# Performance work log

Measured on AMD Instinct MI355X. Metric: run time of the kernel, lower is better.

## Reference

```python
import jax, jax.numpy as jnp
import numpy as np

H = 12       # num heads
D = 64       # head dim
EPS = 1e-5

def rms_norm(x, eps=EPS):
    var = jnp.mean(jnp.square(x), axis=-1, keepdims=True)
    return x * jax.lax.rsqrt(var + eps)

def rotate_half(x):
    x1, x2 = jnp.split(x, 2, axis=-1)
    return jnp.concatenate([-x2, x1], axis=-1)

def setup_inputs() -> dict:
    key = jax.random.key(0)
    ks = jax.random.split(key, 7)
    B, S, C = 2, 2048, 768
    inter = 2048
    hidden_states = jax.random.normal(ks[0], (B, S, C), dtype=jnp.float32)
    # RoPE tables (cos/sin over positions, standard half-duplicated freqs)
    theta = 10000.0
    inv_freq = 1.0 / (theta ** (jnp.arange(0, D, 2, dtype=jnp.float32) / D))
    t = jnp.arange(S, dtype=jnp.float32)
    freqs = jnp.outer(t, inv_freq)            # [S, D/2]
    emb = jnp.concatenate([freqs, freqs], -1)  # [S, D]
    cos = jnp.cos(emb)
    sin = jnp.sin(emb)
    s = 0.02
    w_qkv = jax.random.normal(ks[1], (3 * H * D, C), dtype=jnp.float32) * s
    w_o = jax.random.normal(ks[2], (C, H * D), dtype=jnp.float32) * s
    w_gate_up = jax.random.normal(ks[3], (2 * inter, C), dtype=jnp.float32) * s
    w_down = jax.random.normal(ks[4], (C, inter), dtype=jnp.float32) * s
    return {"hidden_states": hidden_states, "cos": cos, "sin": sin,
            "w_qkv": w_qkv, "w_o": w_o, "w_gate_up": w_gate_up, "w_down": w_down}

def reference(hidden_states, cos, sin, w_qkv, w_o, w_gate_up, w_down):
    B, S, C = hidden_states.shape
    scale = 1.0 / jnp.sqrt(jnp.asarray(D, hidden_states.dtype))
    # ----- attention (manual, non-flash) -----
    qkv = jnp.einsum('bsc,ec->bse', hidden_states, w_qkv)
    qkv = qkv.reshape(B, S, 3 * H, D)
    q, k, v = qkv[:, :, :H], qkv[:, :, H:2 * H], qkv[:, :, 2 * H:]
    c = cos[None, :, None, :]
    sn = sin[None, :, None, :]
    q = q * c + rotate_half(q) * sn
    k = k * c + rotate_half(k) * sn
    scores = jnp.einsum('bihd,bjhd->bhij', q, k) * scale  # [B,H,S,S]
    attn = jax.nn.softmax(scores, axis=-1)
    ctx = jnp.einsum('bhij,bjhd->bihd', attn, v).reshape(B, S, H * D)
    attn_out = jnp.einsum('bse,ce->bsc', ctx, w_o)
    x = rms_norm(hidden_states + attn_out)
    # ----- SwiGLU MLP -----
    gu = jnp.einsum('bsc,ec->bse', x, w_gate_up)
    gate, up = jnp.split(gu, 2, axis=-1)
    mlp_out = jnp.einsum('bsi,ci->bsc', jax.nn.silu(gate) * up, w_down)
    return rms_norm(x + mlp_out)
```

## Files before the change

### kernel.cpp

```cpp
#include <hip/hip_runtime.h>


typedef __attribute__((ext_vector_type(8))) __bf16 bf16x8;
typedef __attribute__((ext_vector_type(8))) short short8;
typedef __attribute__((ext_vector_type(4))) short short4v;
typedef __attribute__((ext_vector_type(4))) float f32x4;
typedef __attribute__((ext_vector_type(4))) float float4v;
typedef __attribute__((ext_vector_type(4))) unsigned int u32x4;

#define CDIM   768
#define HEADS  12
#define DH     64
#define SEQ    2048
#define BATCH  2
#define MROWS  4096
#define QKV_N  2304
#define INTER  2048
#define GU_N   4096
#define NSPLIT 4
#define KCHUNK (SEQ / NSPLIT)
#define BH     (BATCH * HEADS)

#define QSCALE 0.18033688011112043f

static __device__ __forceinline__ unsigned short f2bf(float f) {
  unsigned int u = __builtin_bit_cast(unsigned int, f);
  u += 0x7fffu + ((u >> 16) & 1u);
  return (unsigned short)(u >> 16);
}
static __device__ __forceinline__ float bf2f(unsigned short u) {
  return __builtin_bit_cast(float, ((unsigned int)u) << 16);
}

static __device__ __forceinline__ bf16x8 ld8(const unsigned short* p) {
  return __builtin_bit_cast(bf16x8, *reinterpret_cast<const short8*>(p));
}

static __device__ __forceinline__ float exp2_raw(float x) {
  float r; asm("v_exp_f32 %0, %1" : "=v"(r) : "v"(x)); return r;
}
static __device__ __forceinline__ unsigned cvtpk(float lo, float hi) {
  unsigned r;
  asm("v_cvt_pk_bf16_f32 %0, %1, %2" : "=v"(r) : "v"(lo), "v"(hi));
  return r;
}

static __device__ __forceinline__ void pl32swap(unsigned& a, unsigned& b) {
  auto r = __builtin_amdgcn_permlane32_swap(a, b, false, false);
  a = r[0]; b = r[1];
}
static __device__ __forceinline__ void pl16swap(unsigned& a, unsigned& b) {
  auto r = __builtin_amdgcn_permlane16_swap(a, b, false, false);
  a = r[0]; b = r[1];
}
static __device__ __forceinline__ float red32max(float x) {
  unsigned xi = __builtin_bit_cast(unsigned, x);
  auto r = __builtin_amdgcn_permlane32_swap(xi, xi, false, false);
  return fmaxf(__builtin_bit_cast(float, r[0]), __builtin_bit_cast(float, r[1]));
}
static __device__ __forceinline__ float red16max(float x) {
  unsigned xi = __builtin_bit_cast(unsigned, x);
  auto r = __builtin_amdgcn_permlane16_swap(xi, xi, false, false);
  return fmaxf(__builtin_bit_cast(float, r[0]), __builtin_bit_cast(float, r[1]));
}
static __device__ __forceinline__ float red32sum(float x) {
  unsigned xi = __builtin_bit_cast(unsigned, x);
  auto r = __builtin_amdgcn_permlane32_swap(xi, xi, false, false);
  return __builtin_bit_cast(float, r[0]) + __builtin_bit_cast(float, r[1]);
}
static __device__ __forceinline__ float red16sum(float x) {
  unsigned xi = __builtin_bit_cast(unsigned, x);
  auto r = __builtin_amdgcn_permlane16_swap(xi, xi, false, false);
  return __builtin_bit_cast(float, r[0]) + __builtin_bit_cast(float, r[1]);
}

__global__ __launch_bounds__(256) void cast_all(
    const float* __restrict__ h, const float* __restrict__ wqkv,
    const float* __restrict__ wo, const float* __restrict__ wgu,
    const float* __restrict__ wd,
    unsigned short* __restrict__ hb, unsigned short* __restrict__ wqkvb,
    unsigned short* __restrict__ wob, unsigned short* __restrict__ wgub,
    unsigned short* __restrict__ wdb) {
  const int n0 = 786432, n1 = 442368, n2 = 147456, n3 = 786432, n4 = 393216;
  const int total = n0 + n1 + n2 + n3 + n4;
  for (int i = blockIdx.x * blockDim.x + threadIdx.x; i < total;
       i += gridDim.x * blockDim.x) {
    int j = i;
    const float* src; unsigned short* dst;
    if      (j < n0)            { src = h;    dst = hb;    }
    else if ((j -= n0) < n1)    { src = wqkv; dst = wqkvb; }
    else if ((j -= n1) < n2)    { src = wo;   dst = wob;   }
    else if ((j -= n2) < n3)    { src = wgu;  dst = wgub;  }
    else    { j -= n3;            src = wd;   dst = wdb;   }
    float4v v = *reinterpret_cast<const float4v*>(src + 4 * (size_t)j);
    short4v o;
#pragma unroll
    for (int e = 0; e < 4; ++e) o[e] = (short)f2bf(v[e]);
    *reinterpret_cast<short4v*>(dst + 4 * (size_t)j) = o;
  }
}

template <int BN, bool BF16OUT>
__global__ __launch_bounds__(256) void gemm_lds(
    const unsigned short* __restrict__ A, const unsigned short* __restrict__ W,
    void* __restrict__ Cout, int Mm, int Nn, int Kk) {
  constexpr int MR = (BN == 128) ? 4 : 2;
  __shared__ unsigned short Alds[4096];
  __shared__ unsigned short Blds[BN * 32];
  const int t = threadIdx.x;
  const int lane = t & 63, w = t >> 6;
  const int lr = lane & 15, lg = lane >> 4;
  const int row0 = blockIdx.y * 128, col0 = blockIdx.x * BN;
  const int wrb = (BN == 128) ? (w >> 1) * 64 : w * 32;
  const int wcb = (BN == 128) ? (w & 1) * 64 : 0;

  const unsigned short* ga = A + (size_t)(row0 + (t >> 2)) * Kk + (t & 3) * 8;
  const unsigned short* gb = W + (size_t)(col0 + (t >> 2)) * Kk + (t & 3) * 8;
  const size_t g64 = (size_t)64 * Kk;
  unsigned short* la0 = Alds + w * 512;
  unsigned short* lb0 = Blds + w * 512;
  const unsigned short* ra = Alds + (wrb + lr) * 32 + lg * 8;
  const unsigned short* rb = Blds + (wcb + lr) * 32 + lg * 8;

  f32x4 acc[MR][4] = {};
  for (int k0 = 0; k0 < Kk; k0 += 32) {
    __builtin_amdgcn_global_load_lds((const unsigned int*)(ga + k0),
                                     (unsigned int*)la0, 16, 0, 0);
    __builtin_amdgcn_global_load_lds((const unsigned int*)(ga + k0 + g64),
                                     (unsigned int*)(la0 + 2048), 16, 0, 0);
    __builtin_amdgcn_global_load_lds((const unsigned int*)(gb + k0),
                                     (unsigned int*)lb0, 16, 0, 0);
    if constexpr (BN == 128)
      __builtin_amdgcn_global_load_lds((const unsigned int*)(gb + k0 + g64),
                                       (unsigned int*)(lb0 + 2048), 16, 0, 0);
    __syncthreads();
    bf16x8 af[MR], bfr[4];
#pragma unroll
    for (int m = 0; m < MR; ++m) af[m] = ld8(ra + m * 512);
#pragma unroll
    for (int n = 0; n < 4; ++n) bfr[n] = ld8(rb + n * 512);
    __builtin_amdgcn_s_setprio(1);
#pragma unroll
    for (int m = 0; m < MR; ++m)
#pragma unroll
      for (int n = 0; n < 4; ++n)
        acc[m][n] = __builtin_amdgcn_mfma_f32_16x16x32_bf16(af[m], bfr[n],
                                                            acc[m][n], 0, 0, 0);
    __builtin_amdgcn_s_setprio(0);
    __syncthreads();
  }
#pragma unroll
  for (int m = 0; m < MR; ++m)
#pragma unroll
    for (int j = 0; j < 4; ++j) {
      const size_t roff = (size_t)(row0 + wrb + m * 16 + lg * 4 + j) * Nn +
                          col0 + wcb + lr;
      if constexpr (BF16OUT) {
        unsigned short* cr = (unsigned short*)Cout + roff;
#pragma unroll
        for (int n = 0; n < 4; ++n) cr[n * 16] = f2bf(acc[m][n][j]);
      } else {
        float* cr = (float*)Cout + roff;
#pragma unroll
        for (int n = 0; n < 4; ++n) cr[n * 16] = acc[m][n][j];
      }
    }
}

__global__ __launch_bounds__(256) void rope_qk(
    const unsigned short* __restrict__ qkv, const float* __restrict__ cosT,
    const float* __restrict__ sinT, unsigned short* __restrict__ qtile,
    unsigned short* __restrict__ ktile) {
  const int row = blockIdx.x * 4 + (threadIdx.x >> 6);
  const int d = threadIdx.x & 63;
  const int hh = row % 24;
  const int bs = row / 24;
  const int s = bs & (SEQ - 1);
  const int b = bs >> 11;
  float v = bf2f(qkv[(size_t)bs * QKV_N + hh * 64 + d]);
  float partner = __shfl_xor(v, 32, 64);
  float rot = (d < 32) ? -partner : partner;
  v = v * cosT[s * 64 + d] + rot * sinT[s * 64 + d];
  const int t = s >> 4, lr = s & 15;
  const int dh = d >> 5, lg = (d & 31) >> 3, j = d & 7;
  if (hh < 12) {
    const int bh = b * HEADS + hh;
    qtile[((size_t)(bh * 128 + t) * 2 + dh) * 512 + (lg * 16 + lr) * 8 + j] =
        f2bf(v * QSCALE);
  } else {
    const int bh = b * HEADS + (hh - 12);
    ktile[((size_t)(bh * 128 + t) * 2 + dh) * 512 + (lg * 16 + lr) * 8 + j] =
        f2bf(v);
  }
}

__global__ __launch_bounds__(256) void v_trans(
    const unsigned short* __restrict__ qkv, unsigned short* __restrict__ vT) {
  __shared__ unsigned short tile[64][66];
  const int bh = blockIdx.x;
  const int s0 = blockIdx.y * 64;
  const int b = bh / HEADS, h = bh % HEADS;
  const unsigned short* src = qkv + ((size_t)(b * SEQ + s0)) * QKV_N + (24 + h) * 64;
  const int d = threadIdx.x & 63, sg = threadIdx.x >> 6;
#pragma unroll
  for (int i = 0; i < 16; ++i) {
    int s = sg * 16 + i;
    tile[s][d] = src[(size_t)s * QKV_N + d];
  }
  __syncthreads();
  const int lane = threadIdx.x & 63, wid = threadIdx.x >> 6;
  const int lr = lane & 15, lg = lane >> 4;
  unsigned short* dst = vT + ((size_t)bh * 64 + (s0 >> 5)) * 4 * 512;
#pragma unroll
  for (int tt = 0; tt < 2; ++tt) {
    const int ti = wid * 2 + tt;
    const int kt = ti >> 2, d0 = (ti & 3) * 16;
    short8 o;
#pragma unroll
    for (int j = 0; j < 8; ++j)
      o[j] = (short)tile[kt * 32 + lg * 8 + j][d0 + lr];
    *reinterpret_cast<short8*>(dst + ((size_t)kt * 4 + (ti & 3)) * 512 +
                               lane * 8) = o;
  }
}

__global__ __launch_bounds__(256) void attn_fused(
    const unsigned short* __restrict__ qtile, const unsigned short* __restrict__ ktile,
    const unsigned short* __restrict__ vtile, unsigned short* __restrict__ ctxp,
    float2* __restrict__ ml) {
  const int lane = threadIdx.x & 63, wid = threadIdx.x >> 6;
  const int tid = blockIdx.x * 4 + wid;
  const int sp = tid & 3;
  const int qt = (tid >> 2) & 127;
  const int bh = tid >> 9;
  const int lr = lane & 15, lg = lane >> 4;

  const unsigned short* qp =
      qtile + ((size_t)(bh * 128 + qt) * 2) * 512 + lane * 8;
  bf16x8 qf0 = ld8(qp);
  bf16x8 qf1 = ld8(qp + 512);
  const unsigned short* kb = ktile + (size_t)bh * 128 * 2 * 512 + lane * 8;
  const unsigned short* vb = vtile + (size_t)bh * 64 * 4 * 512 + lane * 8;

  f32x4 acc0 = {0,0,0,0}, acc1 = {0,0,0,0}, acc2 = {0,0,0,0}, acc3 = {0,0,0,0};
  float m = -1e30f, l_lane = 0.f;

  for (int k0 = sp * KCHUNK; k0 < sp * KCHUNK + KCHUNK; k0 += 64) {
    const unsigned short* kp = kb + (size_t)(k0 >> 4) * 1024;
    f32x4 st0 = {0,0,0,0}, st1 = {0,0,0,0}, st2 = {0,0,0,0}, st3 = {0,0,0,0};
    __builtin_amdgcn_s_setprio(1);
    st0 = __builtin_amdgcn_mfma_f32_16x16x32_bf16(ld8(kp),        qf0, st0, 0,0,0);
    st0 = __builtin_amdgcn_mfma_f32_16x16x32_bf16(ld8(kp + 512),  qf1, st0, 0,0,0);
    st1 = __builtin_amdgcn_mfma_f32_16x16x32_bf16(ld8(kp + 1024), qf0, st1, 0,0,0);
    st1 = __builtin_amdgcn_mfma_f32_16x16x32_bf16(ld8(kp + 1536), qf1, st1, 0,0,0);
    st2 = __builtin_amdgcn_mfma_f32_16x16x32_bf16(ld8(kp + 2048), qf0, st2, 0,0,0);
    st2 = __builtin_amdgcn_mfma_f32_16x16x32_bf16(ld8(kp + 2560), qf1, st2, 0,0,0);
    st3 = __builtin_amdgcn_mfma_f32_16x16x32_bf16(ld8(kp + 3072), qf0, st3, 0,0,0);
    st3 = __builtin_amdgcn_mfma_f32_16x16x32_bf16(ld8(kp + 3584), qf1, st3, 0,0,0);
    __builtin_amdgcn_s_setprio(0);

    float tmax = fmaxf(
        fmaxf(fmaxf(fmaxf(st0[0], st0[1]), fmaxf(st0[2], st0[3])),
              fmaxf(fmaxf(st1[0], st1[1]), fmaxf(st1[2], st1[3]))),
        fmaxf(fmaxf(fmaxf(st2[0], st2[1]), fmaxf(st2[2], st2[3])),
              fmaxf(fmaxf(st3[0], st3[1]), fmaxf(st3[2], st3[3]))));
    tmax = red16max(red32max(tmax));

    if (tmax > m + 11.0f) {
      float fac = exp2_raw(m - tmax);
      m = tmax;
      l_lane *= fac;
      acc0 *= fac; acc1 *= fac; acc2 *= fac; acc3 *= fac;
    }

    float p[16];
#pragma unroll
    for (int r = 0; r < 4; ++r) {
      p[r]      = exp2_raw(st0[r] - m);
      p[4 + r]  = exp2_raw(st1[r] - m);
      p[8 + r]  = exp2_raw(st2[r] - m);
      p[12 + r] = exp2_raw(st3[r] - m);
    }
    l_lane += (((p[0] + p[1]) + (p[2] + p[3])) +
               ((p[4] + p[5]) + (p[6] + p[7]))) +
              (((p[8] + p[9]) + (p[10] + p[11])) +
               ((p[12] + p[13]) + (p[14] + p[15])));

    unsigned c0 = cvtpk(p[0], p[1]),   c1 = cvtpk(p[2], p[3]);
    unsigned c2 = cvtpk(p[4], p[5]),   c3 = cvtpk(p[6], p[7]);
    unsigned c4 = cvtpk(p[8], p[9]),   c5 = cvtpk(p[10], p[11]);
    unsigned c6 = cvtpk(p[12], p[13]), c7 = cvtpk(p[14], p[15]);
    pl32swap(c0, c2); pl32swap(c1, c3); pl16swap(c0, c2); pl16swap(c1, c3);
    pl32swap(c4, c6); pl32swap(c5, c7); pl16swap(c4, c6); pl16swap(c5, c7);
    u32x4 pw0 = {c0, c1, c2, c3};
    u32x4 pw1 = {c4, c5, c6, c7};
    bf16x8 pf0 = __builtin_bit_cast(bf16x8, pw0);
    bf16x8 pf1 = __builtin_bit_cast(bf16x8, pw1);

    const unsigned short* vp = vb + (size_t)(k0 >> 5) * 2048;
    __builtin_amdgcn_s_setprio(1);
    acc0 = __builtin_amdgcn_mfma_f32_16x16x32_bf16(ld8(vp),        pf0, acc0, 0,0,0);
    acc1 = __builtin_amdgcn_mfma_f32_16x16x32_bf16(ld8(vp + 512),  pf0, acc1, 0,0,0);
    acc2 = __builtin_amdgcn_mfma_f32_16x16x32_bf16(ld8(vp + 1024), pf0, acc2, 0,0,0);
    acc3 = __builtin_amdgcn_mfma_f32_16x16x32_bf16(ld8(vp + 1536), pf0, acc3, 0,0,0);
    acc0 = __builtin_amdgcn_mfma_f32_16x16x32_bf16(ld8(vp + 2048), pf1, acc0, 0,0,0);
    acc1 = __builtin_amdgcn_mfma_f32_16x16x32_bf16(ld8(vp + 2560), pf1, acc1, 0,0,0);
    acc2 = __builtin_amdgcn_mfma_f32_16x16x32_bf16(ld8(vp + 3072), pf1, acc2, 0,0,0);
    acc3 = __builtin_amdgcn_mfma_f32_16x16x32_bf16(ld8(vp + 3584), pf1, acc3, 0,0,0);
    __builtin_amdgcn_s_setprio(0);
  }

  const float l = red16sum(red32sum(l_lane));

  unsigned short* pp = ctxp +
      (((size_t)(sp * BH + bh)) * SEQ + qt * 16 + lr) * DH + 4 * lg;
  short4v o0, o1, o2, o3;
#pragma unroll
  for (int r = 0; r < 4; ++r) {
    o0[r] = (short)f2bf(acc0[r]);
    o1[r] = (short)f2bf(acc1[r]);
    o2[r] = (short)f2bf(acc2[r]);
    o3[r] = (short)f2bf(acc3[r]);
  }
  *reinterpret_cast<short4v*>(pp)      = o0;
  *reinterpret_cast<short4v*>(pp + 16) = o1;
  *reinterpret_cast<short4v*>(pp + 32) = o2;
  *reinterpret_cast<short4v*>(pp + 48) = o3;
  if (lane < 16) {
    float2 v; v.x = m; v.y = l;
    ml[(size_t)sp * (BH * SEQ) + bh * SEQ + qt * 16 + lr] = v;
  }
}

__global__ __launch_bounds__(256) void attn_combine(
    const unsigned short* __restrict__ ctxp, const float2* __restrict__ ml,
    unsigned short* __restrict__ ctx) {
  const int idx = blockIdx.x * 256 + threadIdx.x;
  const int d = idx & 63;
  const int row = idx >> 6;
  float m0 = ml[row].x,                 l0 = ml[row].y;
  float m1 = ml[row + BH*SEQ].x,        l1 = ml[row + BH*SEQ].y;
  float m2 = ml[row + 2*BH*SEQ].x,      l2 = ml[row + 2*BH*SEQ].y;
  float m3 = ml[row + 3*BH*SEQ].x,      l3 = ml[row + 3*BH*SEQ].y;
  float M = fmaxf(fmaxf(m0, m1), fmaxf(m2, m3));
  float w0 = exp2_raw(m0 - M), w1 = exp2_raw(m1 - M);
  float w2 = exp2_raw(m2 - M), w3 = exp2_raw(m3 - M);
  float den = w0 * l0 + w1 * l1 + w2 * l2 + w3 * l3;
  const size_t pstride = (size_t)BH * SEQ * DH;
  float num = w0 * bf2f(ctxp[(size_t)row * DH + d]) +
              w1 * bf2f(ctxp[(size_t)row * DH + d + pstride]) +
              w2 * bf2f(ctxp[(size_t)row * DH + d + 2 * pstride]) +
              w3 * bf2f(ctxp[(size_t)row * DH + d + 3 * pstride]);
  const int bh = row >> 11, s = row & (SEQ - 1);
  const int b = bh / HEADS, h = bh % HEADS;
  ctx[((size_t)(b * SEQ + s)) * CDIM + h * DH + d] = f2bf(num / den);
}

__global__ __launch_bounds__(256) void add_rmsnorm(
    const float* __restrict__ a, const float* __restrict__ b,
    float* __restrict__ outf, unsigned short* __restrict__ outb) {
  const int row = blockIdx.x;
  const int tid = threadIdx.x;
  const float* ap = a + (size_t)row * CDIM;
  const float* bp = b + (size_t)row * CDIM;
  float v0 = ap[tid]       + bp[tid];
  float v1 = ap[tid + 256] + bp[tid + 256];
  float v2 = ap[tid + 512] + bp[tid + 512];
  float ss = v0 * v0 + v1 * v1 + v2 * v2;
#pragma unroll
  for (int off = 32; off > 0; off >>= 1) ss += __shfl_xor(ss, off, 64);
  __shared__ float red[4];
  if ((tid & 63) == 0) red[tid >> 6] = ss;
  __syncthreads();
  float tot = red[0] + red[1] + red[2] + red[3];
  float r = rsqrtf(tot * (1.f / 768.f) + 1e-5f);
  float* of = outf + (size_t)row * CDIM;
  of[tid]       = v0 * r;
  of[tid + 256] = v1 * r;
  of[tid + 512] = v2 * r;
  if (outb) {
    unsigned short* ob = outb + (size_t)row * CDIM;
    ob[tid]       = f2bf(v0 * r);
    ob[tid + 256] = f2bf(v1 * r);
    ob[tid + 512] = f2bf(v2 * r);
  }
}

__global__ __launch_bounds__(256) void silu_mul(
    const unsigned short* __restrict__ gu, unsigned short* __restrict__ hb) {
  const int i = blockIdx.x * 256 + threadIdx.x;
  const int s = i >> 11, c = i & (INTER - 1);
  float g = bf2f(gu[(size_t)s * GU_N + c]);
  float u = bf2f(gu[(size_t)s * GU_N + INTER + c]);
  float sig = 1.f / (1.f + __expf(-g));
  hb[i] = f2bf(g * sig * u);
}

extern "C" void kernel_launch(void* const* d_in, const int* in_sizes, int n_in,
                              void* d_out, int out_size, void* d_ws, size_t ws_size,
                              hipStream_t stream) {
  const float* hidden = (const float*)d_in[0];
  const float* cosT   = (const float*)d_in[1];
  const float* sinT   = (const float*)d_in[2];
  const float* wqkv   = (const float*)d_in[3];
  const float* wo     = (const float*)d_in[4];
  const float* wgu    = (const float*)d_in[5];
  const float* wd     = (const float*)d_in[6];
  float* out = (float*)d_out;

  char* wsp = (char*)d_ws;
  size_t off = 0;
  auto alloc = [&](size_t bytes) { void* p = wsp + off; off += bytes; return p; };

  unsigned short* wqkvb = (unsigned short*)alloc(2ull * 1769472);
  unsigned short* wob   = (unsigned short*)alloc(2ull * 589824);
  unsigned short* wgub  = (unsigned short*)alloc(2ull * 3145728);
  unsigned short* wdb   = (unsigned short*)alloc(2ull * 1572864);
  unsigned short* hb    = (unsigned short*)alloc(2ull * 3145728);
  float*          x     = (float*)alloc(4ull * 3145728);
  unsigned short* xb    = (unsigned short*)alloc(2ull * 3145728);
  const size_t roff = off;

  unsigned short* qkvb = (unsigned short*)alloc(2ull * MROWS * QKV_N);
  unsigned short* qT   = (unsigned short*)alloc(2ull * MROWS * CDIM);
  unsigned short* kT   = (unsigned short*)alloc(2ull * MROWS * CDIM);
  unsigned short* vTb  = (unsigned short*)alloc(2ull * MROWS * CDIM);
  unsigned short* ctx  = (unsigned short*)alloc(2ull * MROWS * CDIM);
  float*          attn = (float*)alloc(4ull * MROWS * CDIM);
  unsigned short* ctxp = (unsigned short*)alloc(2ull * NSPLIT * BH * SEQ * DH);
  float2*         ml   = (float2*)alloc(8ull * NSPLIT * BH * SEQ);

  off = roff;
  unsigned short* gub  = (unsigned short*)alloc(2ull * MROWS * GU_N);
  unsigned short* hmid = (unsigned short*)alloc(2ull * MROWS * INTER);
  float*          mlp  = (float*)alloc(4ull * MROWS * CDIM);
  (void)ws_size; (void)in_sizes; (void)n_in; (void)out_size;

  cast_all<<<2048, 256, 0, stream>>>(hidden, wqkv, wo, wgu, wd,
                                     hb, wqkvb, wob, wgub, wdb);
  gemm_lds<128, true><<<dim3(QKV_N / 128, MROWS / 128), 256, 0, stream>>>(
      hb, wqkvb, qkvb, MROWS, QKV_N, CDIM);
  rope_qk<<<(MROWS * 24) / 4, 256, 0, stream>>>(qkvb, cosT, sinT, qT, kT);
  v_trans<<<dim3(BH, SEQ / 64), 256, 0, stream>>>(qkvb, vTb);
  attn_fused<<<(BH * (SEQ / 16) * NSPLIT) / 4, 256, 0, stream>>>(
      qT, kT, vTb, ctxp, ml);
  attn_combine<<<(BH * SEQ * DH) / 256, 256, 0, stream>>>(ctxp, ml, ctx);
  gemm_lds<64, false><<<dim3(CDIM / 64, MROWS / 128), 256, 0, stream>>>(
      ctx, wob, attn, MROWS, CDIM, CDIM);
  add_rmsnorm<<<MROWS, 256, 0, stream>>>(hidden, attn, x, xb);
  gemm_lds<128, true><<<dim3(GU_N / 128, MROWS / 128), 256, 0, stream>>>(
      xb, wgub, gub, MROWS, GU_N, CDIM);
  silu_mul<<<(MROWS * INTER) / 256, 256, 0, stream>>>(gub, hmid);
  gemm_lds<64, false><<<dim3(CDIM / 64, MROWS / 128), 256, 0, stream>>>(
      hmid, wdb, mlp, MROWS, CDIM, INTER);
  add_rmsnorm<<<MROWS, 256, 0, stream>>>(x, mlp, out, nullptr);
}
```

Baseline: 349.4 us.

## Process two query tiles per wave in attention to reuse K/V fragments

Each wave in the fused attention kernel now handles two 16-row query tiles instead of one. The K and V fragments for each 64-key step are loaded into registers once and shared by both tiles, which halves global/L2 traffic for K/V per query, and the grid is halved to match. Running two independent softmax chains also gives the scheduler more MFMA and exp work to interleave. The cost is higher register pressure (16 fragment registers plus doubled accumulators), which may lower occupancy, and fewer waves in total.

```diff
diff --git a/kernel.cpp b/kernel.cpp
--- a/kernel.cpp
+++ b/kernel.cpp
@@ -231,104 +231,178 @@
   const int lane = threadIdx.x & 63, wid = threadIdx.x >> 6;
   const int tid = blockIdx.x * 4 + wid;
   const int sp = tid & 3;
-  const int qt = (tid >> 2) & 127;
-  const int bh = tid >> 9;
+  const int qtp = (tid >> 2) & 63;
+  const int bh = tid >> 8;
   const int lr = lane & 15, lg = lane >> 4;
+  const int qt0 = qtp * 2, qt1 = qt0 + 1;
 
   const unsigned short* qp =
-      qtile + ((size_t)(bh * 128 + qt) * 2) * 512 + lane * 8;
-  bf16x8 qf0 = ld8(qp);
-  bf16x8 qf1 = ld8(qp + 512);
+      qtile + ((size_t)(bh * 128 + qt0) * 2) * 512 + lane * 8;
+  bf16x8 qA0 = ld8(qp);
+  bf16x8 qA1 = ld8(qp + 512);
+  bf16x8 qB0 = ld8(qp + 1024);
+  bf16x8 qB1 = ld8(qp + 1536);
   const unsigned short* kb = ktile + (size_t)bh * 128 * 2 * 512 + lane * 8;
   const unsigned short* vb = vtile + (size_t)bh * 64 * 4 * 512 + lane * 8;
 
-  f32x4 acc0 = {0,0,0,0}, acc1 = {0,0,0,0}, acc2 = {0,0,0,0}, acc3 = {0,0,0,0};
-  float m = -1e30f, l_lane = 0.f;
+  f32x4 aA0 = {0,0,0,0}, aA1 = {0,0,0,0}, aA2 = {0,0,0,0}, aA3 = {0,0,0,0};
+  f32x4 aB0 = {0,0,0,0}, aB1 = {0,0,0,0}, aB2 = {0,0,0,0}, aB3 = {0,0,0,0};
+  float mA = -1e30f, mB = -1e30f, lA = 0.f, lB = 0.f;
 
   for (int k0 = sp * KCHUNK; k0 < sp * KCHUNK + KCHUNK; k0 += 64) {
     const unsigned short* kp = kb + (size_t)(k0 >> 4) * 1024;
-    f32x4 st0 = {0,0,0,0}, st1 = {0,0,0,0}, st2 = {0,0,0,0}, st3 = {0,0,0,0};
+    const unsigned short* vp = vb + (size_t)(k0 >> 5) * 2048;
+    bf16x8 kf[8], vf[8];
+#pragma unroll
+    for (int i = 0; i < 8; ++i) kf[i] = ld8(kp + i * 512);
+#pragma unroll
+    for (int i = 0; i < 8; ++i) vf[i] = ld8(vp + i * 512);
+
+    f32x4 sA0 = {0,0,0,0}, sA1 = {0,0,0,0}, sA2 = {0,0,0,0}, sA3 = {0,0,0,0};
+    f32x4 sB0 = {0,0,0,0}, sB1 = {0,0,0,0}, sB2 = {0,0,0,0}, sB3 = {0,0,0,0};
     __builtin_amdgcn_s_setprio(1);
-    st0 = __builtin_amdgcn_mfma_f32_16x16x32_bf16(ld8(kp),        qf0, st0, 0,0,0);
-    st0 = __builtin_amdgcn_mfma_f32_16x16x32_bf16(ld8(kp + 512),  qf1, st0, 0,0,0);
-    st1 = __builtin_amdgcn_mfma_f32_16x16x32_bf16(ld8(kp + 1024), qf0, st1, 0,0,0);
-    st1 = __builtin_amdgcn_mfma_f32_16x16x32_bf16(ld8(kp + 1536), qf1, st1, 0,0,0);
-    st2 = __builtin_amdgcn_mfma_f32_16x16x32_bf16(ld8(kp + 2048), qf0, st2, 0,0,0);
-    st2 = __builtin_amdgcn_mfma_f32_16x16x32_bf16(ld8(kp + 2560), qf1, st2, 0,0,0);
-    st3 = __builtin_amdgcn_mfma_f32_16x16x32_bf16(ld8(kp + 3072), qf0, st3, 0,0,0);
-    st3 = __builtin_amdgcn_mfma_f32_16x16x32_bf16(ld8(kp + 3584), qf1, st3, 0,0,0);
+    sA0 = __builtin_amdgcn_mfma_f32_16x16x32_bf16(kf[0], qA0, sA0, 0,0,0);
+    sA0 = __builtin_amdgcn_mfma_f32_16x16x32_bf16(kf[1], qA1, sA0, 0,0,0);
+    sA1 = __builtin_amdgcn_mfma_f32_16x16x32_bf16(kf[2], qA0, sA1, 0,0,0);
+    sA1 = __builtin_amdgcn_mfma_f32_16x16x32_bf16(kf[3], qA1, sA1, 0,0,0);
+    sA2 = __builtin_amdgcn_mfma_f32_16x16x32_bf16(kf[4], qA0, sA2, 0,0,0);
+    sA2 = __builtin_amdgcn_mfma_f32_16x16x32_bf16(kf[5], qA1, sA2, 0,0,0);
+    sA3 = __builtin_amdgcn_mfma_f32_16x16x32_bf16(kf[6], qA0, sA3, 0,0,0);
+    sA3 = __builtin_amdgcn_mfma_f32_16x16x32_bf16(kf[7], qA1, sA3, 0,0,0);
+    sB0 = __builtin_amdgcn_mfma_f32_16x16x32_bf16(kf[0], qB0, sB0, 0,0,0);
+    sB0 = __builtin_amdgcn_mfma_f32_16x16x32_bf16(kf[1], qB1, sB0, 0,0,0);
+    sB1 = __builtin_amdgcn_mfma_f32_16x16x32_bf16(kf[2], qB0, sB1, 0,0,0);
+    sB1 = __builtin_amdgcn_mfma_f32_16x16x32_bf16(kf[3], qB1, sB1, 0,0,0);
+    sB2 = __builtin_amdgcn_mfma_f32_16x16x32_bf16(kf[4], qB0, sB2, 0,0,0);
+    sB2 = __builtin_amdgcn_mfma_f32_16x16x32_bf16(kf[5], qB1, sB2, 0,0,0);
+    sB3 = __builtin_amdgcn_mfma_f32_16x16x32_bf16(kf[6], qB0, sB3, 0,0,0);
+    sB3 = __builtin_amdgcn_mfma_f32_16x16x32_bf16(kf[7], qB1, sB3, 0,0,0);
     __builtin_amdgcn_s_setprio(0);
 
-    float tmax = fmaxf(
-        fmaxf(fmaxf(fmaxf(st0[0], st0[1]), fmaxf(st0[2], st0[3])),
-              fmaxf(fmaxf(st1[0], st1[1]), fmaxf(st1[2], st1[3]))),
-        fmaxf(fmaxf(fmaxf(st2[0], st2[1]), fmaxf(st2[2], st2[3])),
-              fmaxf(fmaxf(st3[0], st3[1]), fmaxf(st3[2], st3[3]))));
-    tmax = red16max(red32max(tmax));
-
-    if (tmax > m + 11.0f) {
-      float fac = exp2_raw(m - tmax);
-      m = tmax;
-      l_lane *= fac;
-      acc0 *= fac; acc1 *= fac; acc2 *= fac; acc3 *= fac;
-    }
-
-    float p[16];
+    bf16x8 pfA0, pfA1, pfB0, pfB1;
+    {
+      float tmax = fmaxf(
+          fmaxf(fmaxf(fmaxf(sA0[0], sA0[1]), fmaxf(sA0[2], sA0[3])),
+                fmaxf(fmaxf(sA1[0], sA1[1]), fmaxf(sA1[2], sA1[3]))),
+          fmaxf(fmaxf(fmaxf(sA2[0], sA2[1]), fmaxf(sA2[2], sA2[3])),
+                fmaxf(fmaxf(sA3[0], sA3[1]), fmaxf(sA3[2], sA3[3]))));
+      tmax = red16max(red32max(tmax));
+      if (tmax > mA + 11.0f) {
+        float fac = exp2_raw(mA - tmax);
+        mA = tmax; lA *= fac;
+        aA0 *= fac; aA1 *= fac; aA2 *= fac; aA3 *= fac;
+      }
+      float p[16];
+#pragma unroll
+      for (int r = 0; r < 4; ++r) {
+        p[r]      = exp2_raw(sA0[r] - mA);
+        p[4 + r]  = exp2_raw(sA1[r] - mA);
+        p[8 + r]  = exp2_raw(sA2[r] - mA);
+        p[12 + r] = exp2_raw(sA3[r] - mA);
+      }
+      lA += (((p[0]+p[1])+(p[2]+p[3])) + ((p[4]+p[5])+(p[6]+p[7]))) +
+            (((p[8]+p[9])+(p[10]+p[11])) + ((p[12]+p[13])+(p[14]+p[15])));
+      unsigned c0 = cvtpk(p[0], p[1]),   c1 = cvtpk(p[2], p[3]);
+      unsigned c2 = cvtpk(p[4], p[5]),   c3 = cvtpk(p[6], p[7]);
+      unsigned c4 = cvtpk(p[8], p[9]),   c5 = cvtpk(p[10], p[11]);
+      unsigned c6 = cvtpk(p[12], p[13]), c7 = cvtpk(p[14], p[15]);
+      pl32swap(c0, c2); pl32swap(c1, c3); pl16swap(c0, c2); pl16swap(c1, c3);
+      pl32swap(c4, c6); pl32swap(c5, c7); pl16swap(c4, c6); pl16swap(c5, c7);
+      u32x4 w0 = {c0, c1, c2, c3}, w1 = {c4, c5, c6, c7};
+      pfA0 = __builtin_bit_cast(bf16x8, w0);
+      pfA1 = __builtin_bit_cast(bf16x8, w1);
+    }
+    {
+      float tmax = fmaxf(
+          fmaxf(fmaxf(fmaxf(sB0[0], sB0[1]), fmaxf(sB0[2], sB0[3])),
+                fmaxf(fmaxf(sB1[0], sB1[1]), fmaxf(sB1[2], sB1[3]))),
+          fmaxf(fmaxf(fmaxf(sB2[0], sB2[1]), fmaxf(sB2[2], sB2[3])),
+                fmaxf(fmaxf(sB3[0], sB3[1]), fmaxf(sB3[2], sB3[3]))));
+      tmax = red16max(red32max(tmax));
+      if (tmax > mB + 11.0f) {
+        float fac = exp2_raw(mB - tmax);
+        mB = tmax; lB *= fac;
+        aB0 *= fac; aB1 *= fac; aB2 *= fac; aB3 *= fac;
+      }
+      float p[16];
+#pragma unroll
+      for (int r = 0; r < 4; ++r) {
+        p[r]      = exp2_raw(sB0[r] - mB);
+        p[4 + r]  = exp2_raw(sB1[r] - mB);
+        p[8 + r]  = exp2_raw(sB2[r] - mB);
+        p[12 + r] = exp2_raw(sB3[r] - mB);
+      }
+      lB += (((p[0]+p[1])+(p[2]+p[3])) + ((p[4]+p[5])+(p[6]+p[7]))) +
+            (((p[8]+p[9])+(p[10]+p[11])) + ((p[12]+p[13])+(p[14]+p[15])));
+      unsigned c0 = cvtpk(p[0], p[1]),   c1 = cvtpk(p[2], p[3]);
+      unsigned c2 = cvtpk(p[4], p[5]),   c3 = cvtpk(p[6], p[7]);
+      unsigned c4 = cvtpk(p[8], p[9]),   c5 = cvtpk(p[10], p[11]);
+      unsigned c6 = cvtpk(p[12], p[13]), c7 = cvtpk(p[14], p[15]);
+      pl32swap(c0, c2); pl32swap(c1, c3); pl16swap(c0, c2); pl16swap(c1, c3);
+      pl32swap(c4, c6); pl32swap(c5, c7); pl16swap(c4, c6); pl16swap(c5, c7);
+      u32x4 w0 = {c0, c1, c2, c3}, w1 = {c4, c5, c6, c7};
+      pfB0 = __builtin_bit_cast(bf16x8, w0);
+      pfB1 = __builtin_bit_cast(bf16x8, w1);
+    }
+
+    __builtin_amdgcn_s_setprio(1);
+    aA0 = __builtin_amdgcn_mfma_f32_16x16x32_bf16(vf[0], pfA0, aA0, 0,0,0);
+    aA1 = __builtin_amdgcn_mfma_f32_16x16x32_bf16(vf[1], pfA0, aA1, 0,0,0);
+    aA2 = __builtin_amdgcn_mfma_f32_16x16x32_bf16(vf[2], pfA0, aA2, 0,0,0);
+    aA3 = __builtin_amdgcn_mfma_f32_16x16x32_bf16(vf[3], pfA0, aA3, 0,0,0);
+    aA0 = __builtin_amdgcn_mfma_f32_16x16x32_bf16(vf[4], pfA1, aA0, 0,0,0);
+    aA1 = __builtin_amdgcn_mfma_f32_16x16x32_bf16(vf[5], pfA1, aA1, 0,0,0);
+    aA2 = __builtin_amdgcn_mfma_f32_16x16x32_bf16(vf[6], pfA1, aA2, 0,0,0);
+    aA3 = __builtin_amdgcn_mfma_f32_16x16x32_bf16(vf[7], pfA1, aA3, 0,0,0);
+    aB0 = __builtin_amdgcn_mfma_f32_16x16x32_bf16(vf[0], pfB0, aB0, 0,0,0);
+    aB1 = __builtin_amdgcn_mfma_f32_16x16x32_bf16(vf[1], pfB0, aB1, 0,0,0);
+    aB2 = __builtin_amdgcn_mfma_f32_16x16x32_bf16(vf[2], pfB0, aB2, 0,0,0);
+    aB3 = __builtin_amdgcn_mfma_f32_16x16x32_bf16(vf[3], pfB0, aB3, 0,0,0);
+    aB0 = __builtin_amdgcn_mfma_f32_16x16x32_bf16(vf[4], pfB1, aB0, 0,0,0);
+    aB1 = __builtin_amdgcn_mfma_f32_16x16x32_bf16(vf[5], pfB1, aB1, 0,0,0);
+    aB2 = __builtin_amdgcn_mfma_f32_16x16x32_bf16(vf[6], pfB1, aB2, 0,0,0);
+    aB3 = __builtin_amdgcn_mfma_f32_16x16x32_bf16(vf[7], pfB1, aB3, 0,0,0);
+    __builtin_amdgcn_s_setprio(0);
+  }
+
+  const float lAr = red16sum(red32sum(lA));
+  const float lBr = red16sum(red32sum(lB));
+
+  {
+    unsigned short* pp = ctxp +
+        (((size_t)(sp * BH + bh)) * SEQ + qt0 * 16 + lr) * DH + 4 * lg;
+    short4v o0, o1, o2, o3;
 #pragma unroll
     for (int r = 0; r < 4; ++r) {
-      p[r]      = exp2_raw(st0[r] - m);
-      p[4 + r]  = exp2_raw(st1[r] - m);
-      p[8 + r]  = exp2_raw(st2[r] - m);
-      p[12 + r] = exp2_raw(st3[r] - m);
-    }
-    l_lane += (((p[0] + p[1]) + (p[2] + p[3])) +
-               ((p[4] + p[5]) + (p[6] + p[7]))) +
-              (((p[8] + p[9]) + (p[10] + p[11])) +
-               ((p[12] + p[13]) + (p[14] + p[15])));
-
-    unsigned c0 = cvtpk(p[0], p[1]),   c1 = cvtpk(p[2], p[3]);
-    unsigned c2 = cvtpk(p[4], p[5]),   c3 = cvtpk(p[6], p[7]);
-    unsigned c4 = cvtpk(p[8], p[9]),   c5 = cvtpk(p[10], p[11]);
-    unsigned c6 = cvtpk(p[12], p[13]), c7 = cvtpk(p[14], p[15]);
-    pl32swap(c0, c2); pl32swap(c1, c3); pl16swap(c0, c2); pl16swap(c1, c3);
-    pl32swap(c4, c6); pl32swap(c5, c7); pl16swap(c4, c6); pl16swap(c5, c7);
-    u32x4 pw0 = {c0, c1, c2, c3};
-    u32x4 pw1 = {c4, c5, c6, c7};
-    bf16x8 pf0 = __builtin_bit_cast(bf16x8, pw0);
-    bf16x8 pf1 = __builtin_bit_cast(bf16x8, pw1);
-
-    const unsigned short* vp = vb + (size_t)(k0 >> 5) * 2048;
-    __builtin_amdgcn_s_setprio(1);
-    acc0 = __builtin_amdgcn_mfma_f32_16x16x32_bf16(ld8(vp),        pf0, acc0, 0,0,0);
-    acc1 = __builtin_amdgcn_mfma_f32_16x16x32_bf16(ld8(vp + 512),  pf0, acc1, 0,0,0);
-    acc2 = __builtin_amdgcn_mfma_f32_16x16x32_bf16(ld8(vp + 1024), pf0, acc2, 0,0,0);
-    acc3 = __builtin_amdgcn_mfma_f32_16x16x32_bf16(ld8(vp + 1536), pf0, acc3, 0,0,0);
-    acc0 = __builtin_amdgcn_mfma_f32_16x16x32_bf16(ld8(vp + 2048), pf1, acc0, 0,0,0);
-    acc1 = __builtin_amdgcn_mfma_f32_16x16x32_bf16(ld8(vp + 2560), pf1, acc1, 0,0,0);
-    acc2 = __builtin_amdgcn_mfma_f32_16x16x32_bf16(ld8(vp + 3072), pf1, acc2, 0,0,0);
-    acc3 = __builtin_amdgcn_mfma_f32_16x16x32_bf16(ld8(vp + 3584), pf1, acc3, 0,0,0);
-    __builtin_amdgcn_s_setprio(0);
-  }
-
-  const float l = red16sum(red32sum(l_lane));
-
-  unsigned short* pp = ctxp +
-      (((size_t)(sp * BH + bh)) * SEQ + qt * 16 + lr) * DH + 4 * lg;
-  short4v o0, o1, o2, o3;
-#pragma unroll
-  for (int r = 0; r < 4; ++r) {
-    o0[r] = (short)f2bf(acc0[r]);
-    o1[r] = (short)f2bf(acc1[r]);
-    o2[r] = (short)f2bf(acc2[r]);
-    o3[r] = (short)f2bf(acc3[r]);
-  }
-  *reinterpret_cast<short4v*>(pp)      = o0;
-  *reinterpret_cast<short4v*>(pp + 16) = o1;
-  *reinterpret_cast<short4v*>(pp + 32) = o2;
-  *reinterpret_cast<short4v*>(pp + 48) = o3;
-  if (lane < 16) {
-    float2 v; v.x = m; v.y = l;
-    ml[(size_t)sp * (BH * SEQ) + bh * SEQ + qt * 16 + lr] = v;
+      o0[r] = (short)f2bf(aA0[r]); o1[r] = (short)f2bf(aA1[r]);
+      o2[r] = (short)f2bf(aA2[r]); o3[r] = (short)f2bf(aA3[r]);
+    }
+    *reinterpret_cast<short4v*>(pp)      = o0;
+    *reinterpret_cast<short4v*>(pp + 16) = o1;
+    *reinterpret_cast<short4v*>(pp + 32) = o2;
+    *reinterpret_cast<short4v*>(pp + 48) = o3;
+    if (lane < 16) {
+      float2 v; v.x = mA; v.y = lAr;
+      ml[(size_t)sp * (BH * SEQ) + bh * SEQ + qt0 * 16 + lr] = v;
+    }
+  }
+  {
+    unsigned short* pp = ctxp +
+        (((size_t)(sp * BH + bh)) * SEQ + qt1 * 16 + lr) * DH + 4 * lg;
+    short4v o0, o1, o2, o3;
+#pragma unroll
+    for (int r = 0; r < 4; ++r) {
+      o0[r] = (short)f2bf(aB0[r]); o1[r] = (short)f2bf(aB1[r]);
+      o2[r] = (short)f2bf(aB2[r]); o3[r] = (short)f2bf(aB3[r]);
+    }
+    *reinterpret_cast<short4v*>(pp)      = o0;
+    *reinterpret_cast<short4v*>(pp + 16) = o1;
+    *reinterpret_cast<short4v*>(pp + 32) = o2;
+    *reinterpret_cast<short4v*>(pp + 48) = o3;
+    if (lane < 16) {
+      float2 v; v.x = mB; v.y = lBr;
+      ml[(size_t)sp * (BH * SEQ) + bh * SEQ + qt1 * 16 + lr] = v;
+    }
   }
 }
 
@@ -442,7 +516,7 @@
       hb, wqkvb, qkvb, MROWS, QKV_N, CDIM);
   rope_qk<<<(MROWS * 24) / 4, 256, 0, stream>>>(qkvb, cosT, sinT, qT, kT);
   v_trans<<<dim3(BH, SEQ / 64), 256, 0, stream>>>(qkvb, vTb);
-  attn_fused<<<(BH * (SEQ / 16) * NSPLIT) / 4, 256, 0, stream>>>(
+  attn_fused<<<(BH * (SEQ / 32) * NSPLIT) / 4, 256, 0, stream>>>(
       qT, kT, vTb, ctxp, ml);
   attn_combine<<<(BH * SEQ * DH) / 256, 256, 0, stream>>>(ctxp, ml, ctx);
   gemm_lds<64, false><<<dim3(CDIM / 64, MROWS / 128), 256, 0, stream>>>(
```

New measurement: 326.3 us. 1.07x faster.
